# Kernel tuning notes

Hardware: AMD Instinct MI355X
Metric: run time of the kernel (lower is better)

The kernel has to match this reference:

```python
import jax, jax.numpy as jnp
import numpy as np

_CLIP_MIN = 1e-06
_POS_ALPHA = 0.001
NUM_CLASSES = 26
RADIUS = 3
POOL = 3  # rmi_pool_size == rmi_pool_stride
HALF_D = RADIUS * RADIUS


def _max_pool2d(x):
    # torch F.max_pool2d(kernel=3, stride=3, padding=1): pads with -inf
    return jax.lax.reduce_window(
        x, -jnp.inf, jax.lax.max,
        window_dimensions=(1, 1, POOL, POOL),
        window_strides=(1, 1, POOL, POOL),
        padding=[(0, 0), (0, 0), (1, 1), (1, 1)])


def _get_pairs(x):
    # stack radius^2 shifted views: [n,c,H,W] -> [n,c,half_d,new_h,new_w]
    h, w = x.shape[2], x.shape[3]
    nh, nw = h - (RADIUS - 1), w - (RADIUS - 1)
    views = [x[:, :, y:y + nh, xx:xx + nw] for y in range(RADIUS) for xx in range(RADIUS)]
    return jnp.stack(views, axis=2)


def _log_det_by_cholesky(m):
    chol = jnp.linalg.cholesky(m)
    diag = jnp.diagonal(chol, axis1=-2, axis2=-1)
    return 2.0 * jnp.sum(jnp.log(diag + 1e-08), axis=-1)


def _rmi_lower_bound(labels_4D, probs_4D):
    labels_4D = _max_pool2d(labels_4D)
    probs_4D = _max_pool2d(probs_4D)
    n, c = labels_4D.shape[0], labels_4D.shape[1]
    la = _get_pairs(labels_4D).reshape(n, c, HALF_D, -1)  # [n,c,9,M]
    pr = _get_pairs(probs_4D).reshape(n, c, HALF_D, -1)
    eye = jnp.eye(HALF_D, dtype=pr.dtype)
    la = la - jnp.mean(la, axis=3, keepdims=True)
    pr = pr - jnp.mean(pr, axis=3, keepdims=True)
    la_cov = jnp.einsum('ncdm,ncem->ncde', la, la)
    pr_cov = jnp.einsum('ncdm,ncem->ncde', pr, pr)
    pr_cov_inv = jnp.linalg.inv(pr_cov + eye * _POS_ALPHA)
    la_pr_cov = jnp.einsum('ncdm,ncem->ncde', la, pr)
    appro_var = la_cov - jnp.einsum('ncde,ncef,ncgf->ncdg', la_pr_cov, pr_cov_inv, la_pr_cov)
    rmi_now = 0.5 * _log_det_by_cholesky(appro_var + eye * _POS_ALPHA)  # [n,c]
    rmi_per_class = jnp.mean(rmi_now.reshape(-1, NUM_CLASSES), axis=0) / float(HALF_D)
    return jnp.sum(rmi_per_class)


def setup_inputs() -> dict:
    key = jax.random.key(0)
    k1, k2, k3 = jax.random.split(key, 3)
    n, c, h, w = 4, NUM_CLASSES, 512, 512
    cls_score = jax.random.normal(k1, (n, c, h, w), dtype=jnp.float32)
    new_targets = jax.random.randint(k2, (n, c, h, w), 0, 2).astype(jnp.float32)
    valid_indices = jax.random.randint(k3, (n, h, w), 0, 2).astype(jnp.float32)
    return {"cls_score": cls_score, "new_targets": new_targets, "valid_indices": valid_indices}


def reference(cls_score, new_targets, valid_indices):
    mask = valid_indices[:, None, :, :]  # [n,1,h,w]
    valid_onehot = new_targets * mask
    probs = jax.nn.sigmoid(cls_score) * mask + _CLIP_MIN
    return _rmi_lower_bound(valid_onehot, probs)
```

## Files before the change

kernel.cpp:

```cpp
#include <hip/hip_runtime.h>
#include <math.h>

#define NUM_CLASSES 26
#define HH 512
#define WW 512
#define NB 4
#define PHH 171
#define PWW 171
#define NHH 169
#define NWW 169
#define MPTS (NHH*NWW)
#define NCT (NB*NUM_CLASSES)
#define CLIPV 1e-6f
#define PSTR 176
#define NCHUNK 8
#define ROWS_PER_CHUNK 22
#define NSLOT 189

__global__ __launch_bounds__(256) void pool_kernel(const float* __restrict__ cls,
        const float* __restrict__ tgt, const float* __restrict__ mask,
        float* __restrict__ poolL, float* __restrict__ poolP) {
    __shared__ float amax[4][512];
    __shared__ float lmax[4][512];
    const int w = threadIdx.x >> 6, lane = threadIdx.x & 63;
    const int R = blockIdx.x * 4 + w;
    const int ph = R % PHH, nc = R / PHH, n = nc / NUM_CLASSES;

    const float4* c4 = (const float4*)(cls  + (size_t)nc * HH * WW);
    const float4* t4 = (const float4*)(tgt  + (size_t)nc * HH * WW);
    const float4* m4 = (const float4*)(mask + (size_t)n  * HH * WW);

    float am[8], lm[8];
    #pragma unroll
    for (int k = 0; k < 8; ++k) { am[k] = -INFINITY; lm[k] = 0.f; }

    const int r0 = 3 * ph - 1;
    const int s0 = (ph == 0) ? 1 : 0;
    for (int s = s0; s < 3; ++s) {
        int rbase = (r0 + s) * 128;
        #pragma unroll
        for (int g = 0; g < 2; ++g) {
            int i4 = rbase + lane + 64 * g;
            float4 c = c4[i4];
            float4 t = t4[i4];
            float4 m = m4[i4];
            float cc[4] = {c.x, c.y, c.z, c.w};
            float tt[4] = {t.x, t.y, t.z, t.w};
            float mm[4] = {m.x, m.y, m.z, m.w};
            #pragma unroll
            for (int k = 0; k < 4; ++k) {
                int j = 4 * g + k;
                am[j] = fmaxf(am[j], mm[k] > 0.5f ? cc[k] : -INFINITY);
                lm[j] = fmaxf(lm[j], tt[k] * mm[k]);
            }
        }
    }
    *(float4*)&amax[w][4 * lane]       = make_float4(am[0], am[1], am[2], am[3]);
    *(float4*)&amax[w][256 + 4 * lane] = make_float4(am[4], am[5], am[6], am[7]);
    *(float4*)&lmax[w][4 * lane]       = make_float4(lm[0], lm[1], lm[2], lm[3]);
    *(float4*)&lmax[w][256 + 4 * lane] = make_float4(lm[4], lm[5], lm[6], lm[7]);
    __syncthreads();

    const size_t rowo = (size_t)(nc * PHH + ph) * PSTR;
    #pragma unroll
    for (int j = 0; j < 3; ++j) {
        int pw = lane + 64 * j;
        if (pw < PWW) {
            int cM = 3 * pw;
            float a = fmaxf(amax[w][cM], amax[w][cM + 1]);
            float l = fmaxf(lmax[w][cM], lmax[w][cM + 1]);
            if (cM > 0) {
                a = fmaxf(a, amax[w][cM - 1]);
                l = fmaxf(l, lmax[w][cM - 1]);
            }
            poolP[rowo + pw] = __fdividef(1.0f, 1.0f + __expf(-a)) + CLIPV;
            poolL[rowo + pw] = (l > 0.5f) ? 1.0f : 0.0f;
        } else if (j == 2 && lane >= 43 && lane < 48) {
            int pc = 128 + lane;
            poolP[rowo + pc] = 0.f;
            poolL[rowo + pc] = 0.f;
        }
    }
}

__global__ __launch_bounds__(256, 4) void cov_kernel(const float* __restrict__ poolL,
        const float* __restrict__ poolP, float* __restrict__ partial) {
    const int nc = blockIdx.x, mode = blockIdx.y, ch = blockIdx.z;
    const int tid = threadIdx.x, lane = tid & 63, wave = tid >> 6;
    const int rowbase = ch * ROWS_PER_CHUNK;
    const int rc = (rowbase + ROWS_PER_CHUNK <= NHH) ? ROWS_PER_CHUNK : (NHH - rowbase);
    const float* Lb = poolL + (size_t)nc * PHH * PSTR;
    const float* Pb = poolP + (size_t)nc * PHH * PSTR;
    const int items = rc * 43;

    __shared__ float red[4][54];

    if (mode < 2) {
        const float* src = mode ? Pb : Lb;
        float acc[45], sm[9];
        #pragma unroll
        for (int k = 0; k < 45; ++k) acc[k] = 0.f;
        #pragma unroll
        for (int k = 0; k < 9; ++k) sm[k] = 0.f;

        for (int it = tid; it < items; it += 256) {
            int i  = rowbase + it / 43;
            int j0 = (it - (it / 43) * 43) * 4;
            const float* rp = src + (size_t)i * PSTR + j0;
            float4 x0 = *(const float4*)(rp);
            float4 x1 = *(const float4*)(rp + 4);
            float4 y0 = *(const float4*)(rp + PSTR);
            float4 y1 = *(const float4*)(rp + PSTR + 4);
            float4 z0 = *(const float4*)(rp + 2 * PSTR);
            float4 z1 = *(const float4*)(rp + 2 * PSTR + 4);
            float r0[8] = {x0.x, x0.y, x0.z, x0.w, x1.x, x1.y, x1.z, x1.w};
            float r1[8] = {y0.x, y0.y, y0.z, y0.w, y1.x, y1.y, y1.z, y1.w};
            float r2[8] = {z0.x, z0.y, z0.z, z0.w, z1.x, z1.y, z1.z, z1.w};
            #pragma unroll
            for (int q = 0; q < 4; ++q) {
                float sel = (j0 + q < NWW) ? 1.f : 0.f;
                float v[9], vs[9];
                v[0] = r0[q]; v[1] = r0[q + 1]; v[2] = r0[q + 2];
                v[3] = r1[q]; v[4] = r1[q + 1]; v[5] = r1[q + 2];
                v[6] = r2[q]; v[7] = r2[q + 1]; v[8] = r2[q + 2];
                #pragma unroll
                for (int d = 0; d < 9; ++d) { vs[d] = v[d] * sel; sm[d] += vs[d]; }
                int k = 0;
                #pragma unroll
                for (int d = 0; d < 9; ++d)
                    #pragma unroll
                    for (int e = d; e < 9; ++e)
                        acc[k++] += vs[d] * v[e];
            }
        }
        #pragma unroll
        for (int k = 0; k < 45; ++k) {
            float x = acc[k];
            #pragma unroll
            for (int off = 32; off > 0; off >>= 1) x += __shfl_down(x, off);
            if (lane == 0) red[wave][k] = x;
        }
        #pragma unroll
        for (int k = 0; k < 9; ++k) {
            float x = sm[k];
            #pragma unroll
            for (int off = 32; off > 0; off >>= 1) x += __shfl_down(x, off);
            if (lane == 0) red[wave][45 + k] = x;
        }
        __syncthreads();
        if (tid < 54) {
            float x = red[0][tid] + red[1][tid] + red[2][tid] + red[3][tid];
            int slot = (tid < 45) ? (mode == 0 ? 0 : 45) + tid
                                  : (mode == 0 ? 171 : 180) + (tid - 45);
            partial[((size_t)ch * NSLOT + slot) * NCT + nc] = x;
        }
    } else {
        const int nd  = (mode == 2) ? 5 : 4;
        const int dof = (mode == 2) ? 0 : 5;
        float acc[45];
        #pragma unroll
        for (int k = 0; k < 45; ++k) acc[k] = 0.f;

        for (int it = tid; it < items; it += 256) {
            int i  = rowbase + it / 43;
            int j0 = (it - (it / 43) * 43) * 4;
            const float* lp = Lb + (size_t)i * PSTR + j0;
            const float* pp = Pb + (size_t)i * PSTR + j0;
            float4 px0 = *(const float4*)(pp);
            float4 px1 = *(const float4*)(pp + 4);
            float4 py0 = *(const float4*)(pp + PSTR);
            float4 py1 = *(const float4*)(pp + PSTR + 4);
            float4 pz0 = *(const float4*)(pp + 2 * PSTR);
            float4 pz1 = *(const float4*)(pp + 2 * PSTR + 4);
            float pr0[8] = {px0.x, px0.y, px0.z, px0.w, px1.x, px1.y, px1.z, px1.w};
            float pr1[8] = {py0.x, py0.y, py0.z, py0.w, py1.x, py1.y, py1.z, py1.w};
            float pr2[8] = {pz0.x, pz0.y, pz0.z, pz0.w, pz1.x, pz1.y, pz1.z, pz1.w};
            const float* la  = lp + (mode == 2 ? 0 : PSTR);
            const float* lb2 = lp + (mode == 2 ? PSTR : 2 * PSTR);
            float4 la0 = *(const float4*)(la);
            float4 la1 = *(const float4*)(la + 4);
            float4 lb0 = *(const float4*)(lb2);
            float4 lb1 = *(const float4*)(lb2 + 4);
            float lrA[8] = {la0.x, la0.y, la0.z, la0.w, la1.x, la1.y, la1.z, la1.w};
            float lrB[8] = {lb0.x, lb0.y, lb0.z, lb0.w, lb1.x, lb1.y, lb1.z, lb1.w};
            #pragma unroll
            for (int q = 0; q < 4; ++q) {
                float sel = (j0 + q < NWW) ? 1.f : 0.f;
                float vp[9];
                vp[0] = pr0[q]; vp[1] = pr0[q + 1]; vp[2] = pr0[q + 2];
                vp[3] = pr1[q]; vp[4] = pr1[q + 1]; vp[5] = pr1[q + 2];
                vp[6] = pr2[q]; vp[7] = pr2[q + 1]; vp[8] = pr2[q + 2];
                float vl[5];
                if (mode == 2) {
                    vl[0] = lrA[q] * sel; vl[1] = lrA[q + 1] * sel; vl[2] = lrA[q + 2] * sel;
                    vl[3] = lrB[q] * sel; vl[4] = lrB[q + 1] * sel;
                } else {
                    vl[0] = lrA[q + 2] * sel;
                    vl[1] = lrB[q] * sel; vl[2] = lrB[q + 1] * sel; vl[3] = lrB[q + 2] * sel;
                }
                #pragma unroll
                for (int d = 0; d < 5; ++d) {
                    if (d < nd) {
                        #pragma unroll
                        for (int e = 0; e < 9; ++e)
                            acc[d * 9 + e] += vl[d] * vp[e];
                    }
                }
            }
        }
        const int nred = nd * 9;
        #pragma unroll
        for (int k = 0; k < 45; ++k) {
            if (k < nred) {
                float x = acc[k];
                #pragma unroll
                for (int off = 32; off > 0; off >>= 1) x += __shfl_down(x, off);
                if (lane == 0) red[wave][k] = x;
            }
        }
        __syncthreads();
        if (tid < nred) {
            float x = red[0][tid] + red[1][tid] + red[2][tid] + red[3][tid];
            int slot = 90 + (dof * 9) + tid;
            partial[((size_t)ch * NSLOT + slot) * NCT + nc] = x;
        }
    }
}

__global__ __launch_bounds__(128) void solve_kernel(const float* __restrict__ partial,
                                                    double* __restrict__ per_nc) {
    const int nc = blockIdx.x;
    const int tid = threadIdx.x;
    __shared__ double cl[45], cp[45], clp[81], sL[9], sP[9];
    __shared__ double All[81], C[81], Pm[81], X[81], A[81];
    __shared__ double logacc;

    for (int s = tid; s < NSLOT; s += 128) {
        double acc = 0.0;
        for (int ch = 0; ch < NCHUNK; ++ch)
            acc += (double)partial[((size_t)ch * NSLOT + s) * NCT + nc];
        if (s < 45)       cl[s] = acc;
        else if (s < 90)  cp[s - 45] = acc;
        else if (s < 171) clp[s - 90] = acc;
        else if (s < 180) sL[s - 171] = acc;
        else              sP[s - 180] = acc;
    }
    if (tid == 0) logacc = 0.0;
    __syncthreads();

    const double M = (double)MPTS;
    if (tid < 81) {
        int d = tid / 9, e = tid % 9;
        int lo = d < e ? d : e, hi = d < e ? e : d;
        int k = 9 * lo - lo * (lo - 1) / 2 + (hi - lo);
        All[tid] = cl[k] - sL[d] * sL[e] / M;
        C[tid]   = cp[k] - sP[d] * sP[e] / M + (d == e ? 1e-3 : 0.0);
        Pm[tid]  = clp[tid] - sL[d] * sP[e] / M;
    }
    __syncthreads();

    for (int k = 0; k < 9; ++k) {
        if (tid == 0) C[k * 9 + k] = sqrt(fmax(C[k * 9 + k], 1e-30));
        __syncthreads();
        if (tid > k && tid < 9) C[tid * 9 + k] /= C[k * 9 + k];
        __syncthreads();
        if (tid < 81) {
            int i = tid / 9, j = tid % 9;
            if (j > k && i >= j) C[i * 9 + j] -= C[i * 9 + k] * C[j * 9 + k];
        }
        __syncthreads();
    }

    for (int e = 0; e < 9; ++e) {
        if (tid < 9) {
            int d = tid;
            double sum = Pm[d * 9 + e];
            for (int k = 0; k < e; ++k) sum -= C[e * 9 + k] * X[k * 9 + d];
            X[e * 9 + d] = sum / C[e * 9 + e];
        }
        __syncthreads();
    }

    if (tid < 81) {
        int d = tid / 9, g = tid % 9;
        double w = 0.0;
        #pragma unroll
        for (int e = 0; e < 9; ++e) w += X[e * 9 + d] * X[e * 9 + g];
        A[tid] = All[tid] - w + (d == g ? 1e-3 : 0.0);
    }
    __syncthreads();

    for (int k = 0; k < 9; ++k) {
        if (tid == 0) {
            double piv = sqrt(fmax(A[k * 9 + k], 0.0));
            A[k * 9 + k] = piv;
            logacc += log(piv + 1e-8);
        }
        __syncthreads();
        if (tid > k && tid < 9) A[tid * 9 + k] /= A[k * 9 + k];
        __syncthreads();
        if (tid < 81) {
            int i = tid / 9, j = tid % 9;
            if (j > k && i >= j) A[i * 9 + j] -= A[i * 9 + k] * A[j * 9 + k];
        }
        __syncthreads();
    }
    if (tid == 0) per_nc[nc] = logacc;
}

__global__ __launch_bounds__(128) void reduce_kernel(const double* __restrict__ per_nc,
                                                     float* __restrict__ out) {
    int t = threadIdx.x;
    double r = (t < NCT) ? per_nc[t] : 0.0;
    __shared__ double red[128];
    red[t] = r;
    __syncthreads();
    for (int s = 64; s > 0; s >>= 1) {
        if (t < s) red[t] += red[t + s];
        __syncthreads();
    }
    if (t == 0) out[0] = (float)(red[0] / 36.0);
}

extern "C" void kernel_launch(void* const* d_in, const int* in_sizes, int n_in,
                              void* d_out, int out_size, void* d_ws, size_t ws_size,
                              hipStream_t stream) {
    const float* cls  = (const float*)d_in[0];
    const float* tgt  = (const float*)d_in[1];
    const float* mask = (const float*)d_in[2];

    double* per_nc  = (double*)d_ws;
    float*  poolL   = (float*)(per_nc + 128);
    float*  poolP   = poolL + (size_t)NCT * PHH * PSTR;
    float*  partial = poolP + (size_t)NCT * PHH * PSTR;

    pool_kernel<<<NCT * PHH / 4, 256, 0, stream>>>(cls, tgt, mask, poolL, poolP);

    dim3 gcov(NCT, 4, NCHUNK);
    cov_kernel<<<gcov, 256, 0, stream>>>(poolL, poolP, partial);

    solve_kernel<<<NCT, 128, 0, stream>>>(partial, per_nc);

    reduce_kernel<<<1, 128, 0, stream>>>(per_nc, (float*)d_out);
}
```

Baseline: 316.6 us.

## Fuse max-pooling into covariance kernel using shared-memory pooled tiles

Merges the pooling and covariance kernels into one: each block pools a 24-row halo tile of labels and probabilities into LDS, then each of its four waves computes one covariance group from shared memory. This removes the global round trip of the pooled arrays and one kernel launch. In exchange, pooling is recomputed for the two halo rows of each chunk, covariance work per block falls from 256 threads to one 64-lane wave per mode, and the large LDS footprint plus 832 blocks may limit occupancy and parallelism.

```diff
diff --git a/kernel.cpp b/kernel.cpp
--- a/kernel.cpp
+++ b/kernel.cpp
@@ -12,107 +12,106 @@
 #define MPTS (NHH*NWW)
 #define NCT (NB*NUM_CLASSES)
 #define CLIPV 1e-6f
-#define PSTR 176
 #define NCHUNK 8
-#define ROWS_PER_CHUNK 22
+#define RPC 22
 #define NSLOT 189
 
-__global__ __launch_bounds__(256) void pool_kernel(const float* __restrict__ cls,
+__global__ __launch_bounds__(256, 3) void fused_kernel(const float* __restrict__ cls,
         const float* __restrict__ tgt, const float* __restrict__ mask,
-        float* __restrict__ poolL, float* __restrict__ poolP) {
-    __shared__ float amax[4][512];
-    __shared__ float lmax[4][512];
-    const int w = threadIdx.x >> 6, lane = threadIdx.x & 63;
-    const int R = blockIdx.x * 4 + w;
-    const int ph = R % PHH, nc = R / PHH, n = nc / NUM_CLASSES;
+        float* __restrict__ partial) {
+    const int nc = blockIdx.x, ch = blockIdx.y;
+    const int n = nc / NUM_CLASSES;
+    const int lane = threadIdx.x & 63, wave = threadIdx.x >> 6;
+    const int rowbase = ch * RPC;
+    const int rc = (rowbase + RPC <= NHH) ? RPC : (NHH - rowbase);
+    const int trows = rc + 2;
+
+    __shared__ float tP[24][176];
+    __shared__ float tL[24][176];
+    __shared__ float amS[4][512];
+    __shared__ float lmS[4][512];
 
     const float4* c4 = (const float4*)(cls  + (size_t)nc * HH * WW);
     const float4* t4 = (const float4*)(tgt  + (size_t)nc * HH * WW);
     const float4* m4 = (const float4*)(mask + (size_t)n  * HH * WW);
 
-    float am[8], lm[8];
-    #pragma unroll
-    for (int k = 0; k < 8; ++k) { am[k] = -INFINITY; lm[k] = 0.f; }
-
-    const int r0 = 3 * ph - 1;
-    const int s0 = (ph == 0) ? 1 : 0;
-    for (int s = s0; s < 3; ++s) {
-        int rbase = (r0 + s) * 128;
-        #pragma unroll
-        for (int g = 0; g < 2; ++g) {
-            int i4 = rbase + lane + 64 * g;
-            float4 c = c4[i4];
-            float4 t = t4[i4];
-            float4 m = m4[i4];
-            float cc[4] = {c.x, c.y, c.z, c.w};
-            float tt[4] = {t.x, t.y, t.z, t.w};
-            float mm[4] = {m.x, m.y, m.z, m.w};
-            #pragma unroll
-            for (int k = 0; k < 4; ++k) {
-                int j = 4 * g + k;
-                am[j] = fmaxf(am[j], mm[k] > 0.5f ? cc[k] : -INFINITY);
-                lm[j] = fmaxf(lm[j], tt[k] * mm[k]);
-            }
-        }
-    }
-    *(float4*)&amax[w][4 * lane]       = make_float4(am[0], am[1], am[2], am[3]);
-    *(float4*)&amax[w][256 + 4 * lane] = make_float4(am[4], am[5], am[6], am[7]);
-    *(float4*)&lmax[w][4 * lane]       = make_float4(lm[0], lm[1], lm[2], lm[3]);
-    *(float4*)&lmax[w][256 + 4 * lane] = make_float4(lm[4], lm[5], lm[6], lm[7]);
-    __syncthreads();
-
-    const size_t rowo = (size_t)(nc * PHH + ph) * PSTR;
-    #pragma unroll
-    for (int j = 0; j < 3; ++j) {
-        int pw = lane + 64 * j;
-        if (pw < PWW) {
-            int cM = 3 * pw;
-            float a = fmaxf(amax[w][cM], amax[w][cM + 1]);
-            float l = fmaxf(lmax[w][cM], lmax[w][cM + 1]);
-            if (cM > 0) {
-                a = fmaxf(a, amax[w][cM - 1]);
-                l = fmaxf(l, lmax[w][cM - 1]);
-            }
-            poolP[rowo + pw] = __fdividef(1.0f, 1.0f + __expf(-a)) + CLIPV;
-            poolL[rowo + pw] = (l > 0.5f) ? 1.0f : 0.0f;
-        } else if (j == 2 && lane >= 43 && lane < 48) {
-            int pc = 128 + lane;
-            poolP[rowo + pc] = 0.f;
-            poolL[rowo + pc] = 0.f;
-        }
-    }
-}
-
-__global__ __launch_bounds__(256, 4) void cov_kernel(const float* __restrict__ poolL,
-        const float* __restrict__ poolP, float* __restrict__ partial) {
-    const int nc = blockIdx.x, mode = blockIdx.y, ch = blockIdx.z;
-    const int tid = threadIdx.x, lane = tid & 63, wave = tid >> 6;
-    const int rowbase = ch * ROWS_PER_CHUNK;
-    const int rc = (rowbase + ROWS_PER_CHUNK <= NHH) ? ROWS_PER_CHUNK : (NHH - rowbase);
-    const float* Lb = poolL + (size_t)nc * PHH * PSTR;
-    const float* Pb = poolP + (size_t)nc * PHH * PSTR;
+    for (int k = 0; k < 6; ++k) {
+        int tr = wave + 4 * k;
+        if (tr >= trows) break;
+        int ph = rowbase + tr;
+        float am[8], lm[8];
+        #pragma unroll
+        for (int j = 0; j < 8; ++j) { am[j] = -INFINITY; lm[j] = 0.f; }
+        const int r0 = 3 * ph - 1;
+        #pragma unroll
+        for (int s = 0; s < 3; ++s) {
+            int r = r0 + s;
+            r = r < 0 ? 0 : r;
+            int rb = r * 128;
+            #pragma unroll
+            for (int g = 0; g < 2; ++g) {
+                int i4 = rb + lane + 64 * g;
+                float4 c = c4[i4];
+                float4 t = t4[i4];
+                float4 m = m4[i4];
+                float cc[4] = {c.x, c.y, c.z, c.w};
+                float tt[4] = {t.x, t.y, t.z, t.w};
+                float mm[4] = {m.x, m.y, m.z, m.w};
+                #pragma unroll
+                for (int q = 0; q < 4; ++q) {
+                    int j = 4 * g + q;
+                    am[j] = fmaxf(am[j], mm[q] > 0.5f ? cc[q] : -INFINITY);
+                    lm[j] = fmaxf(lm[j], tt[q] * mm[q]);
+                }
+            }
+        }
+        *(float4*)&amS[wave][4 * lane]       = make_float4(am[0], am[1], am[2], am[3]);
+        *(float4*)&amS[wave][256 + 4 * lane] = make_float4(am[4], am[5], am[6], am[7]);
+        *(float4*)&lmS[wave][4 * lane]       = make_float4(lm[0], lm[1], lm[2], lm[3]);
+        *(float4*)&lmS[wave][256 + 4 * lane] = make_float4(lm[4], lm[5], lm[6], lm[7]);
+        #pragma unroll
+        for (int j = 0; j < 3; ++j) {
+            int pw = lane + 64 * j;
+            if (pw < PWW) {
+                int cM = 3 * pw;
+                float a = fmaxf(amS[wave][cM], amS[wave][cM + 1]);
+                float l = fmaxf(lmS[wave][cM], lmS[wave][cM + 1]);
+                if (cM > 0) {
+                    a = fmaxf(a, amS[wave][cM - 1]);
+                    l = fmaxf(l, lmS[wave][cM - 1]);
+                }
+                tP[tr][pw] = __fdividef(1.0f, 1.0f + __expf(-a)) + CLIPV;
+                tL[tr][pw] = (l > 0.5f) ? 1.0f : 0.0f;
+            }
+        }
+        if (lane < 5) {
+            tP[tr][171 + lane] = 0.f;
+            tL[tr][171 + lane] = 0.f;
+        }
+    }
+    __syncthreads();
+
     const int items = rc * 43;
-
-    __shared__ float red[4][54];
-
-    if (mode < 2) {
-        const float* src = mode ? Pb : Lb;
+    float* pbase = partial + (size_t)ch * NSLOT * NCT + nc;
+
+    if (wave < 2) {
+        const float (*src)[176] = wave ? tP : tL;
         float acc[45], sm[9];
         #pragma unroll
         for (int k = 0; k < 45; ++k) acc[k] = 0.f;
         #pragma unroll
         for (int k = 0; k < 9; ++k) sm[k] = 0.f;
 
-        for (int it = tid; it < items; it += 256) {
-            int i  = rowbase + it / 43;
-            int j0 = (it - (it / 43) * 43) * 4;
-            const float* rp = src + (size_t)i * PSTR + j0;
+        for (int it = lane; it < items; it += 64) {
+            int tr = it / 43;
+            int j0 = (it - tr * 43) * 4;
+            const float* rp = &src[tr][j0];
             float4 x0 = *(const float4*)(rp);
             float4 x1 = *(const float4*)(rp + 4);
-            float4 y0 = *(const float4*)(rp + PSTR);
-            float4 y1 = *(const float4*)(rp + PSTR + 4);
-            float4 z0 = *(const float4*)(rp + 2 * PSTR);
-            float4 z1 = *(const float4*)(rp + 2 * PSTR + 4);
+            float4 y0 = *(const float4*)(rp + 176);
+            float4 y1 = *(const float4*)(rp + 180);
+            float4 z0 = *(const float4*)(rp + 352);
+            float4 z1 = *(const float4*)(rp + 356);
             float r0[8] = {x0.x, x0.y, x0.z, x0.w, x1.x, x1.y, x1.z, x1.w};
             float r1[8] = {y0.x, y0.y, y0.z, y0.w, y1.x, y1.y, y1.z, y1.w};
             float r2[8] = {z0.x, z0.y, z0.z, z0.w, z1.x, z1.y, z1.z, z1.w};
@@ -138,45 +137,37 @@
             float x = acc[k];
             #pragma unroll
             for (int off = 32; off > 0; off >>= 1) x += __shfl_down(x, off);
-            if (lane == 0) red[wave][k] = x;
+            if (lane == 0) pbase[(size_t)((wave == 0 ? 0 : 45) + k) * NCT] = x;
         }
         #pragma unroll
         for (int k = 0; k < 9; ++k) {
             float x = sm[k];
             #pragma unroll
             for (int off = 32; off > 0; off >>= 1) x += __shfl_down(x, off);
-            if (lane == 0) red[wave][45 + k] = x;
-        }
-        __syncthreads();
-        if (tid < 54) {
-            float x = red[0][tid] + red[1][tid] + red[2][tid] + red[3][tid];
-            int slot = (tid < 45) ? (mode == 0 ? 0 : 45) + tid
-                                  : (mode == 0 ? 171 : 180) + (tid - 45);
-            partial[((size_t)ch * NSLOT + slot) * NCT + nc] = x;
+            if (lane == 0) pbase[(size_t)((wave == 0 ? 171 : 180) + k) * NCT] = x;
         }
     } else {
-        const int nd  = (mode == 2) ? 5 : 4;
-        const int dof = (mode == 2) ? 0 : 5;
+        const int nd  = (wave == 2) ? 5 : 4;
+        const int dof = (wave == 2) ? 0 : 5;
         float acc[45];
         #pragma unroll
         for (int k = 0; k < 45; ++k) acc[k] = 0.f;
 
-        for (int it = tid; it < items; it += 256) {
-            int i  = rowbase + it / 43;
-            int j0 = (it - (it / 43) * 43) * 4;
-            const float* lp = Lb + (size_t)i * PSTR + j0;
-            const float* pp = Pb + (size_t)i * PSTR + j0;
+        for (int it = lane; it < items; it += 64) {
+            int tr = it / 43;
+            int j0 = (it - tr * 43) * 4;
+            const float* pp = &tP[tr][j0];
             float4 px0 = *(const float4*)(pp);
             float4 px1 = *(const float4*)(pp + 4);
-            float4 py0 = *(const float4*)(pp + PSTR);
-            float4 py1 = *(const float4*)(pp + PSTR + 4);
-            float4 pz0 = *(const float4*)(pp + 2 * PSTR);
-            float4 pz1 = *(const float4*)(pp + 2 * PSTR + 4);
+            float4 py0 = *(const float4*)(pp + 176);
+            float4 py1 = *(const float4*)(pp + 180);
+            float4 pz0 = *(const float4*)(pp + 352);
+            float4 pz1 = *(const float4*)(pp + 356);
             float pr0[8] = {px0.x, px0.y, px0.z, px0.w, px1.x, px1.y, px1.z, px1.w};
             float pr1[8] = {py0.x, py0.y, py0.z, py0.w, py1.x, py1.y, py1.z, py1.w};
             float pr2[8] = {pz0.x, pz0.y, pz0.z, pz0.w, pz1.x, pz1.y, pz1.z, pz1.w};
-            const float* la  = lp + (mode == 2 ? 0 : PSTR);
-            const float* lb2 = lp + (mode == 2 ? PSTR : 2 * PSTR);
+            const float* la  = &tL[tr + (wave == 2 ? 0 : 1)][j0];
+            const float* lb2 = &tL[tr + (wave == 2 ? 1 : 2)][j0];
             float4 la0 = *(const float4*)(la);
             float4 la1 = *(const float4*)(la + 4);
             float4 lb0 = *(const float4*)(lb2);
@@ -191,7 +182,7 @@
                 vp[3] = pr1[q]; vp[4] = pr1[q + 1]; vp[5] = pr1[q + 2];
                 vp[6] = pr2[q]; vp[7] = pr2[q + 1]; vp[8] = pr2[q + 2];
                 float vl[5];
-                if (mode == 2) {
+                if (wave == 2) {
                     vl[0] = lrA[q] * sel; vl[1] = lrA[q + 1] * sel; vl[2] = lrA[q + 2] * sel;
                     vl[3] = lrB[q] * sel; vl[4] = lrB[q + 1] * sel;
                 } else {
@@ -215,14 +206,8 @@
                 float x = acc[k];
                 #pragma unroll
                 for (int off = 32; off > 0; off >>= 1) x += __shfl_down(x, off);
-                if (lane == 0) red[wave][k] = x;
-            }
-        }
-        __syncthreads();
-        if (tid < nred) {
-            float x = red[0][tid] + red[1][tid] + red[2][tid] + red[3][tid];
-            int slot = 90 + (dof * 9) + tid;
-            partial[((size_t)ch * NSLOT + slot) * NCT + nc] = x;
+                if (lane == 0) pbase[(size_t)(90 + dof * 9 + k) * NCT] = x;
+            }
         }
     }
 }
@@ -330,14 +315,10 @@
     const float* mask = (const float*)d_in[2];
 
     double* per_nc  = (double*)d_ws;
-    float*  poolL   = (float*)(per_nc + 128);
-    float*  poolP   = poolL + (size_t)NCT * PHH * PSTR;
-    float*  partial = poolP + (size_t)NCT * PHH * PSTR;
-
-    pool_kernel<<<NCT * PHH / 4, 256, 0, stream>>>(cls, tgt, mask, poolL, poolP);
-
-    dim3 gcov(NCT, 4, NCHUNK);
-    cov_kernel<<<gcov, 256, 0, stream>>>(poolL, poolP, partial);
+    float*  partial = (float*)(per_nc + 128);
+
+    dim3 gfused(NCT, NCHUNK);
+    fused_kernel<<<gfused, 256, 0, stream>>>(cls, tgt, mask, partial);
 
     solve_kernel<<<NCT, 128, 0, stream>>>(partial, per_nc);
 
```

New measurement: 278.0 us. 12.2% less time.
